# Performance work log

Measured on AMD Instinct MI355X. Metric: run time of the kernel, lower is better.

The kernel has to match this reference:

```python
import jax, jax.numpy as jnp
import numpy as np

INPUT_DIM = 384
H1, H2, BOTTLENECK = 512, 216, 10
NUM_ANNOTATORS = 2316
BATCH = 16384


def setup_inputs() -> dict:
    key = jax.random.key(0)
    ks = jax.random.split(key, 9)

    def lin(k, fan_in, fan_out):
        # torch nn.Linear default init: U(-1/sqrt(fan_in), 1/sqrt(fan_in))
        bound = 1.0 / np.sqrt(fan_in)
        kw, kb = jax.random.split(k)
        W = jax.random.uniform(kw, (fan_in, fan_out), jnp.float32, -bound, bound)
        b = jax.random.uniform(kb, (fan_out,), jnp.float32, -bound, bound)
        return W, b

    x = jax.random.normal(ks[0], (BATCH, INPUT_DIM), jnp.float32)
    W1, b1 = lin(ks[1], INPUT_DIM, H1)
    W2, b2 = lin(ks[2], H1, H2)
    W3, b3 = lin(ks[3], H2, BOTTLENECK)
    # 2316 heads of Linear(10, 1) stacked into a single (10, 2316) matrix + (2316,) bias
    Wh, bh = lin(ks[4], BOTTLENECK, NUM_ANNOTATORS)
    return {"x": x, "W1": W1, "b1": b1, "W2": W2, "b2": b2,
            "W3": W3, "b3": b3, "Wh": Wh, "bh": bh}


def reference(x, W1, b1, W2, b2, W3, b3, Wh, bh):
    # shared encoder (dropout is identity in eval mode)
    h = jax.nn.relu(x @ W1 + b1)            # [B, 512]
    h = jax.nn.relu(h @ W2 + b2)            # [B, 216]
    f = jax.nn.relu(h @ W3 + b3)            # [B, 10]
    # 2316 per-annotator heads fused into one GEMM: [B,10] @ [10,2316] + [2316]
    return f @ Wh + bh                      # [B, 2316]
```

## Files before the change

kernel.cpp:

```cpp
#include <hip/hip_runtime.h>
#include <hip/hip_bf16.h>
#include <stdint.h>

using f32x4  = __attribute__((ext_vector_type(4))) float;
using bf16x8 = __attribute__((ext_vector_type(8))) __bf16;
using u16x4  = __attribute__((ext_vector_type(4))) unsigned short;
using u16x8  = __attribute__((ext_vector_type(8))) unsigned short;

#define DEVFN static __device__ __forceinline__

constexpr int IND = 384, N1 = 512, N2R = 216, N2 = 256, NB = 10, NA = 2316;
constexpr int BATCH = 16384;
constexpr int RB  = 64;
constexpr int RBH = 32;
constexpr int NC1 = 12;
constexpr int NC2 = 16;
constexpr int K3  = 224;

constexpr int WS_W1  = 0;
constexpr int WS_W2  = WS_W1 + NC1 * N1 * 32;
constexpr int WS_W3  = WS_W2 + NC2 * N2 * 32;
constexpr int WS_WH  = WS_W3 + 16 * K3;
constexpr int WS_END = WS_WH + NB * NA;
constexpr size_t WS_F_BYTE = 708864;
constexpr size_t WS_NEED   = WS_F_BYTE + (size_t)BATCH * 12 * 4;

constexpr int XT_OFF = 0;      constexpr int XT_ST = 784;
constexpr int W1T    = 51200;
constexpr int H1_OFF = 0;      constexpr int H1_ST = 1040;
constexpr int W2T    = 66560;
constexpr int H2_OFF = 0;      constexpr int H2_ST = 528;
constexpr int W3_OFF = 115712;
constexpr int F_OFF  = 122880; constexpr int F_ST  = 48;
constexpr int B1L    = 149504;
constexpr int B2L    = 151552;
constexpr int B3L    = 152576;
constexpr int LDS_E  = 152640;

DEVFN unsigned short bf16u(float f) {
    __hip_bfloat16 h = __float2bfloat16(f);
    unsigned short u; __builtin_memcpy(&u, &h, 2); return u;
}

DEVFN void mfma16(f32x4& d, bf16x8 a, bf16x8 b) {
    d = __builtin_amdgcn_mfma_f32_16x16x32_bf16(a, b, d, 0, 0, 0);
}

DEVFN void gll16(const void* g, void* lds) {
    __builtin_amdgcn_global_load_lds((const __attribute__((address_space(1))) void*)g,
                                     (__attribute__((address_space(3))) void*)lds, 16, 0, 0);
}

DEVFN void wait_vm4()   { asm volatile("s_waitcnt vmcnt(4)" ::: "memory"); }
DEVFN void wait_vm2()   { asm volatile("s_waitcnt vmcnt(2)" ::: "memory"); }
DEVFN void wait_vm0()   { asm volatile("s_waitcnt vmcnt(0)" ::: "memory"); }
DEVFN void wait_lgkm0() { asm volatile("s_waitcnt lgkmcnt(0)" ::: "memory"); }

__global__ __launch_bounds__(256)
void cvt_weights(const float* __restrict__ W1, const float* __restrict__ W2,
                 const float* __restrict__ W3, const float* __restrict__ Wh,
                 unsigned short* __restrict__ ws)
{
    const int bid = blockIdx.x, tid = threadIdx.x;
    if (bid < 12) {
        const int c = bid;
        #pragma unroll
        for (int half = 0; half < 2; ++half) {
            const int col = half * 256 + tid;
            #pragma unroll
            for (int o = 0; o < 4; ++o) {
                u16x8 v;
                #pragma unroll
                for (int s7 = 0; s7 < 8; ++s7) {
                    int k = c * 32 + o * 8 + s7;
                    v[s7] = bf16u(W1[(size_t)k * N1 + col]);
                }
                *(u16x8*)(ws + WS_W1 + c * 16384 + col * 32 + ((o ^ (col & 3)) << 3)) = v;
            }
        }
    } else if (bid < 28) {
        const int c = bid - 12;
        const int col = tid;
        #pragma unroll
        for (int o = 0; o < 4; ++o) {
            u16x8 v;
            #pragma unroll
            for (int s7 = 0; s7 < 8; ++s7) {
                int k = c * 32 + o * 8 + s7;
                v[s7] = (col < N2R) ? bf16u(W2[(size_t)k * N2R + col]) : (unsigned short)0;
            }
            *(u16x8*)(ws + WS_W2 + c * 8192 + col * 32 + ((o ^ (col & 3)) << 3)) = v;
        }
    } else if (bid == 28) {
        for (int i = tid; i < 16 * K3; i += 256) {
            int col = i / K3, s = i - col * K3;
            int sb = s >> 5, r = s & 31;
            int k = sb * 32 + (((r >> 3) ^ (col & 3)) << 3) + (r & 7);
            float v = (col < NB && k < 216) ? W3[k * NB + col] : 0.f;
            ws[WS_W3 + i] = bf16u(v);
        }
    } else {
        int chunk = (bid - 29) * 256 + tid;
        if (chunk < (NB * NA) / 8) {
            const float4* s = (const float4*)(Wh + chunk * 8);
            float4 p0 = s[0], p1 = s[1];
            u16x8 v;
            v[0]=bf16u(p0.x); v[1]=bf16u(p0.y); v[2]=bf16u(p0.z); v[3]=bf16u(p0.w);
            v[4]=bf16u(p1.x); v[5]=bf16u(p1.y); v[6]=bf16u(p1.z); v[7]=bf16u(p1.w);
            *(u16x8*)(ws + WS_WH + chunk * 8) = v;
        }
    }
}

__global__ __launch_bounds__(512)
void encoder(const float* __restrict__ x,
             const float* __restrict__ b1g, const float* __restrict__ b2g,
             const float* __restrict__ b3g,
             const unsigned short* __restrict__ ws,
             float* __restrict__ fout)
{
    __shared__ __attribute__((aligned(16))) unsigned char smem[LDS_E];
    const int tid  = threadIdx.x;
    const int wave = tid >> 6;
    const int lane = tid & 63;
    const int l16  = lane & 15;
    const int lk   = lane >> 4;
    const int wr   = wave >> 2;
    const int wc   = wave & 3;
    const int row0 = blockIdx.x * RB;

    {
        const float4* xg = (const float4*)(x + (size_t)row0 * IND);
        #pragma unroll
        for (int i = 0; i < 12; ++i) {
            int j = tid + i * 512;
            float4 v = xg[j];
            int el = j * 4, r = el / IND, c = el - r * IND;
            u16x4 h;
            h[0] = bf16u(v.x); h[1] = bf16u(v.y); h[2] = bf16u(v.z); h[3] = bf16u(v.w);
            *(u16x4*)(smem + XT_OFF + r * XT_ST + c * 2) = h;
        }
        *(float*)(smem + B1L + tid * 4) = b1g[tid];
        if (tid < 256) *(float*)(smem + B2L + tid * 4) = (tid < N2R) ? b2g[tid] : 0.f;
        if (tid < 16)  *(float*)(smem + B3L + tid * 4) = (tid < NB)  ? b3g[tid] : 0.f;
    }
    __syncthreads();

    const unsigned char* wsW1 = (const unsigned char*)(ws + WS_W1);
    f32x4 acc1[2][8] = {};

    #pragma unroll
    for (int cc = 0; cc < 2; ++cc)
        #pragma unroll
        for (int o = 0; o < 4; ++o) {
            int wb = o * 8192 + wave * 1024;
            gll16(wsW1 + cc * 32768 + wb + lane * 16, smem + W1T + cc * 32768 + wb);
        }
    for (int c = 0; c < NC1; ++c) {
        if (c + 1 < NC1) wait_vm4(); else wait_vm0();
        __builtin_amdgcn_s_barrier();
        if (c + 2 < NC1) {
            const unsigned char* src = wsW1 + (size_t)(c + 2) * 32768;
            const int nxt = W1T + ((c + 2) % 3) * 32768;
            #pragma unroll
            for (int o = 0; o < 4; ++o) {
                int wb = o * 8192 + wave * 1024;
                gll16(src + wb + lane * 16, smem + nxt + wb);
            }
        }
        const int cur = W1T + (c % 3) * 32768;
        const int k0 = c * 32;
        bf16x8 a0 = *(const bf16x8*)(smem + XT_OFF + (wr * 32 + l16)      * XT_ST + (k0 + lk * 8) * 2);
        bf16x8 a1 = *(const bf16x8*)(smem + XT_OFF + (wr * 32 + 16 + l16) * XT_ST + (k0 + lk * 8) * 2);
        #pragma unroll
        for (int n = 0; n < 8; ++n) {
            int col = wc * 128 + n * 16 + l16;
            bf16x8 b = *(const bf16x8*)(smem + cur + col * 64 + ((lk ^ (col & 3)) << 4));
            mfma16(acc1[0][n], a0, b);
            mfma16(acc1[1][n], a1, b);
        }
    }
    __builtin_amdgcn_s_barrier();
    #pragma unroll
    for (int m = 0; m < 2; ++m)
        #pragma unroll
        for (int n = 0; n < 8; ++n) {
            int col = wc * 128 + n * 16 + l16;
            float bias = *(const float*)(smem + B1L + col * 4);
            #pragma unroll
            for (int e = 0; e < 4; ++e) {
                float v = fmaxf(acc1[m][n][e] + bias, 0.f);
                *(unsigned short*)(smem + H1_OFF + (wr * 32 + m * 16 + lk * 4 + e) * H1_ST + col * 2) = bf16u(v);
            }
        }
    wait_lgkm0();
    __builtin_amdgcn_s_barrier();

    const unsigned char* wsW2 = (const unsigned char*)(ws + WS_W2);
    f32x4 acc2[2][4] = {};

    #pragma unroll
    for (int cc = 0; cc < 2; ++cc)
        #pragma unroll
        for (int o = 0; o < 2; ++o) {
            int wb = o * 8192 + wave * 1024;
            gll16(wsW2 + cc * 16384 + wb + lane * 16, smem + W2T + cc * 16384 + wb);
        }
    for (int c = 0; c < NC2; ++c) {
        if (c + 1 < NC2) wait_vm2(); else wait_vm0();
        __builtin_amdgcn_s_barrier();
        if (c + 2 < NC2) {
            const unsigned char* src = wsW2 + (size_t)(c + 2) * 16384;
            const int nxt = W2T + ((c + 2) % 3) * 16384;
            #pragma unroll
            for (int o = 0; o < 2; ++o) {
                int wb = o * 8192 + wave * 1024;
                gll16(src + wb + lane * 16, smem + nxt + wb);
            }
        }
        const int cur = W2T + (c % 3) * 16384;
        const int k0 = c * 32;
        bf16x8 a0 = *(const bf16x8*)(smem + H1_OFF + (wr * 32 + l16)      * H1_ST + (k0 + lk * 8) * 2);
        bf16x8 a1 = *(const bf16x8*)(smem + H1_OFF + (wr * 32 + 16 + l16) * H1_ST + (k0 + lk * 8) * 2);
        #pragma unroll
        for (int n = 0; n < 4; ++n) {
            int col = wc * 64 + n * 16 + l16;
            bf16x8 b = *(const bf16x8*)(smem + cur + col * 64 + ((lk ^ (col & 3)) << 4));
            mfma16(acc2[0][n], a0, b);
            mfma16(acc2[1][n], a1, b);
        }
    }
    __builtin_amdgcn_s_barrier();
    #pragma unroll
    for (int m = 0; m < 2; ++m)
        #pragma unroll
        for (int n = 0; n < 4; ++n) {
            int col = wc * 64 + n * 16 + l16;
            float bias = *(const float*)(smem + B2L + col * 4);
            #pragma unroll
            for (int e = 0; e < 4; ++e) {
                float v = fmaxf(acc2[m][n][e] + bias, 0.f);
                *(unsigned short*)(smem + H2_OFF + (wr * 32 + m * 16 + lk * 4 + e) * H2_ST + col * 2) = bf16u(v);
            }
        }
    if (wave < 7)
        gll16((const unsigned char*)(ws + WS_W3) + wave * 1024 + lane * 16, smem + W3_OFF + wave * 1024);
    __syncthreads();

    f32x4 acc3[2] = {};
    #pragma unroll
    for (int c = 0; c < 7; ++c) {
        const int k0 = c * 32;
        bf16x8 a0 = *(const bf16x8*)(smem + H2_OFF + (wr * 32 + l16)      * H2_ST + (k0 + lk * 8) * 2);
        bf16x8 a1 = *(const bf16x8*)(smem + H2_OFF + (wr * 32 + 16 + l16) * H2_ST + (k0 + lk * 8) * 2);
        bf16x8 b  = *(const bf16x8*)(smem + W3_OFF + l16 * 448 + c * 64 + ((lk ^ (l16 & 3)) << 4));
        mfma16(acc3[0], a0, b);
        mfma16(acc3[1], a1, b);
    }
    if (wc == 0 && l16 < NB) {
        float bias = *(const float*)(smem + B3L + l16 * 4);
        #pragma unroll
        for (int m = 0; m < 2; ++m)
            #pragma unroll
            for (int e = 0; e < 4; ++e) {
                float v = fmaxf(acc3[m][e] + bias, 0.f);
                *(float*)(smem + F_OFF + (wr * 32 + m * 16 + lk * 4 + e) * F_ST + l16 * 4) = v;
            }
    }
    if (wc == 1 && l16 < 2) {
        #pragma unroll
        for (int m = 0; m < 2; ++m)
            #pragma unroll
            for (int e = 0; e < 4; ++e)
                *(float*)(smem + F_OFF + (wr * 32 + m * 16 + lk * 4 + e) * F_ST + (10 + l16) * 4) = 0.f;
    }
    __syncthreads();

    if (tid < 192)
        *(f32x4*)(fout + (size_t)row0 * 12 + tid * 4) = *(const f32x4*)(smem + F_OFF + tid * 16);
}

__global__ __launch_bounds__(256)
void head(const float* __restrict__ fin, const float* __restrict__ bhg,
          const unsigned short* __restrict__ ws, float* __restrict__ out)
{
    const int tid = threadIdx.x;
    const int r0  = blockIdx.x * RBH;
    const uint2*  __restrict__ WhG = (const uint2*)(ws + WS_WH);
    const float4* __restrict__ bhG = (const float4*)bhg;

    #pragma unroll 1
    for (int rg = 0; rg < 8; ++rg) {
        float fv[4][10];
        #pragma unroll
        for (int rr = 0; rr < 4; ++rr)
            #pragma unroll
            for (int k = 0; k < 10; ++k)
                fv[rr][k] = fin[(size_t)(r0 + rg * 4 + rr) * 12 + k];
        #pragma unroll 1
        for (int j = tid; j < 579; j += 256) {
            float4 bhv = bhG[j];
            float ac[4][4];
            #pragma unroll
            for (int rr = 0; rr < 4; ++rr) {
                ac[rr][0] = bhv.x; ac[rr][1] = bhv.y; ac[rr][2] = bhv.z; ac[rr][3] = bhv.w;
            }
            #pragma unroll
            for (int k = 0; k < 10; ++k) {
                uint2 w = WhG[k * 579 + j];
                float w0 = __uint_as_float(w.x << 16);
                float w1 = __uint_as_float(w.x & 0xffff0000u);
                float w2 = __uint_as_float(w.y << 16);
                float w3 = __uint_as_float(w.y & 0xffff0000u);
                #pragma unroll
                for (int rr = 0; rr < 4; ++rr) {
                    ac[rr][0] = fmaf(fv[rr][k], w0, ac[rr][0]);
                    ac[rr][1] = fmaf(fv[rr][k], w1, ac[rr][1]);
                    ac[rr][2] = fmaf(fv[rr][k], w2, ac[rr][2]);
                    ac[rr][3] = fmaf(fv[rr][k], w3, ac[rr][3]);
                }
            }
            #pragma unroll
            for (int rr = 0; rr < 4; ++rr) {
                float4 o;
                o.x = ac[rr][0]; o.y = ac[rr][1]; o.z = ac[rr][2]; o.w = ac[rr][3];
                *(float4*)(out + (size_t)(r0 + rg * 4 + rr) * NA + j * 4) = o;
            }
        }
    }
}

extern "C" void kernel_launch(void* const* d_in, const int* in_sizes, int n_in,
                              void* d_out, int out_size, void* d_ws, size_t ws_size,
                              hipStream_t stream)
{
    const float* x  = (const float*)d_in[0];
    const float* W1 = (const float*)d_in[1];
    const float* b1 = (const float*)d_in[2];
    const float* W2 = (const float*)d_in[3];
    const float* b2 = (const float*)d_in[4];
    const float* W3 = (const float*)d_in[5];
    const float* b3 = (const float*)d_in[6];
    const float* Wh = (const float*)d_in[7];
    const float* bh = (const float*)d_in[8];
    unsigned short* ws = (unsigned short*)d_ws;
    float* fbuf = (float*)((char*)d_ws + WS_F_BYTE);
    float* out = (float*)d_out;

    if (ws_size < WS_NEED) return;

    cvt_weights<<<dim3(41), dim3(256), 0, stream>>>(W1, W2, W3, Wh, ws);
    encoder<<<dim3(BATCH / RB), dim3(512), 0, stream>>>(x, b1, b2, b3, ws, fbuf);
    head<<<dim3(BATCH / RBH), dim3(256), 0, stream>>>(fbuf, bh, ws, out);
}
```

Before: 61.75 us.

## Split head kernel over column tiles and keep head weights in registers

Restructures the head kernel grid into 3 column tiles × 512 row groups, so each thread loads its 10×4 slice of Wh and the bias into registers once and reuses them across 32 rows. This removes the repeated per-row-group reloads of Wh and bias and the inner column loop, and triples the block count to improve load balance and parallelism. The cost is that the third column tile is mostly idle (579 columns over 768 threads), and the features are re-read from global or cache by every column tile.

```diff
diff --git a/kernel.cpp b/kernel.cpp
--- a/kernel.cpp
+++ b/kernel.cpp
@@ -12,7 +12,6 @@
 constexpr int IND = 384, N1 = 512, N2R = 216, N2 = 256, NB = 10, NA = 2316;
 constexpr int BATCH = 16384;
 constexpr int RB  = 64;
-constexpr int RBH = 32;
 constexpr int NC1 = 12;
 constexpr int NC2 = 16;
 constexpr int K3  = 224;
@@ -285,41 +284,47 @@
           const unsigned short* __restrict__ ws, float* __restrict__ out)
 {
     const int tid = threadIdx.x;
-    const int r0  = blockIdx.x * RBH;
-    const uint2*  __restrict__ WhG = (const uint2*)(ws + WS_WH);
-    const float4* __restrict__ bhG = (const float4*)bhg;
+    const int bid = blockIdx.x;
+    const int jt  = bid >> 9;
+    const int rgt = bid & 511;
+    const int j   = jt * 256 + tid;
+    const bool act = j < 579;
+    const int r0  = rgt * 32;
+
+    float w[10][4];
+    float4 bhv = make_float4(0.f, 0.f, 0.f, 0.f);
+    if (act) {
+        const uint2* __restrict__ WhG = (const uint2*)(ws + WS_WH);
+        #pragma unroll
+        for (int k = 0; k < 10; ++k) {
+            uint2 q = WhG[k * 579 + j];
+            w[k][0] = __uint_as_float(q.x << 16);
+            w[k][1] = __uint_as_float(q.x & 0xffff0000u);
+            w[k][2] = __uint_as_float(q.y << 16);
+            w[k][3] = __uint_as_float(q.y & 0xffff0000u);
+        }
+        bhv = ((const float4*)bhg)[j];
+    }
 
     #pragma unroll 1
     for (int rg = 0; rg < 8; ++rg) {
-        float fv[4][10];
+        const float* __restrict__ fr = fin + (size_t)(r0 + rg * 4) * 12;
+        float ac[4][4];
+        #pragma unroll
+        for (int rr = 0; rr < 4; ++rr) {
+            ac[rr][0] = bhv.x; ac[rr][1] = bhv.y; ac[rr][2] = bhv.z; ac[rr][3] = bhv.w;
+        }
         #pragma unroll
         for (int rr = 0; rr < 4; ++rr)
             #pragma unroll
-            for (int k = 0; k < 10; ++k)
-                fv[rr][k] = fin[(size_t)(r0 + rg * 4 + rr) * 12 + k];
-        #pragma unroll 1
-        for (int j = tid; j < 579; j += 256) {
-            float4 bhv = bhG[j];
-            float ac[4][4];
-            #pragma unroll
-            for (int rr = 0; rr < 4; ++rr) {
-                ac[rr][0] = bhv.x; ac[rr][1] = bhv.y; ac[rr][2] = bhv.z; ac[rr][3] = bhv.w;
-            }
-            #pragma unroll
             for (int k = 0; k < 10; ++k) {
-                uint2 w = WhG[k * 579 + j];
-                float w0 = __uint_as_float(w.x << 16);
-                float w1 = __uint_as_float(w.x & 0xffff0000u);
-                float w2 = __uint_as_float(w.y << 16);
-                float w3 = __uint_as_float(w.y & 0xffff0000u);
-                #pragma unroll
-                for (int rr = 0; rr < 4; ++rr) {
-                    ac[rr][0] = fmaf(fv[rr][k], w0, ac[rr][0]);
-                    ac[rr][1] = fmaf(fv[rr][k], w1, ac[rr][1]);
-                    ac[rr][2] = fmaf(fv[rr][k], w2, ac[rr][2]);
-                    ac[rr][3] = fmaf(fv[rr][k], w3, ac[rr][3]);
-                }
-            }
+                float fv = fr[rr * 12 + k];
+                ac[rr][0] = fmaf(fv, w[k][0], ac[rr][0]);
+                ac[rr][1] = fmaf(fv, w[k][1], ac[rr][1]);
+                ac[rr][2] = fmaf(fv, w[k][2], ac[rr][2]);
+                ac[rr][3] = fmaf(fv, w[k][3], ac[rr][3]);
+            }
+        if (act) {
             #pragma unroll
             for (int rr = 0; rr < 4; ++rr) {
                 float4 o;
@@ -351,5 +356,5 @@
 
     cvt_weights<<<dim3(41), dim3(256), 0, stream>>>(W1, W2, W3, Wh, ws);
     encoder<<<dim3(BATCH / RB), dim3(512), 0, stream>>>(x, b1, b2, b3, ws, fbuf);
-    head<<<dim3(BATCH / RBH), dim3(256), 0, stream>>>(fbuf, bh, ws, out);
-}
+    head<<<dim3(1536), dim3(256), 0, stream>>>(fbuf, bh, ws, out);
+}
```

After: 58.36 us. 5.5% less time.
